# Performance work log

Hardware: AMD Instinct MI355X
Metric: run time of the kernel (lower is better)

## Reference

```python
import jax, jax.numpy as jnp
import numpy as np
from jax import lax

B, T = 8192, 2048
INIT_ALPHA = 0.1


def setup_inputs() -> dict:
    key = jax.random.key(0)
    kx, = jax.random.split(key, 1)
    # intermittent demand: small non-negative integers, many exact zeros
    x = jax.random.randint(kx, (B, T), 0, 3).astype(jnp.float32)
    alpha = jnp.full((1, 1), INIT_ALPHA, dtype=jnp.float32)  # learned smoothing weight
    Z0 = jnp.ones((B,), dtype=jnp.float32)  # demand-size state
    V0 = jnp.ones((B,), dtype=jnp.float32)  # inter-demand-interval state
    q0 = jnp.ones((B,), dtype=jnp.float32)  # periods since last nonzero demand
    return {"x": x, "alpha": alpha, "Z0": Z0, "V0": V0, "q0": q0}


def reference(x, alpha, Z0, V0, q0):
    """Croston's method recurrence (sba=False): out_t = Z_t / V_t.

    x: (B, T) demand series; states are per-series scalars carried through a scan.
    """
    a = alpha[0, 0]

    def step(carry, xt):  # xt: (B,)
        Z, V, q = carry
        Z_next = a * xt + (1.0 - a) * Z
        V_next = a * q + (1.0 - a) * V
        nz = xt != 0.0
        Z_next = jnp.where(nz, Z_next, Z)
        V_next = jnp.where(nz, V_next, V)
        q_next = jnp.where(nz, 1.0, q + 1.0)
        out = Z_next / V_next  # sba=False branch
        return (Z_next, V_next, q_next), out

    _, outs = lax.scan(step, (Z0, V0, q0), x.T)  # outs: (T, B)
    return outs.T  # (B, T)
```

## Files before the change

kernel.cpp:

```cpp
#include <hip/hip_runtime.h>
#include <stdint.h>


#define TLEN 2048

typedef float vf4 __attribute__((ext_vector_type(4)));

__global__ __launch_bounds__(256) void croston_kernel(
    const float* __restrict__ x,
    const float* __restrict__ alpha,
    const float* __restrict__ Z0,
    const float* __restrict__ V0,
    const float* __restrict__ q0,
    float* __restrict__ out)
{
    __shared__ __attribute__((aligned(16))) float lds[4][2048];

    const int warp = threadIdx.x >> 6;
    const int lane = threadIdx.x & 63;
    const int wid  = blockIdx.x * 4 + warp;
    float* W = lds[warp];

    const float a  = alpha[0];
    const float ma = 1.0f - a;

    const int e  = (lane & 7) ^ ((lane >> 3) & 7);
    const int l7 = lane & 7;

    const float* row = x + (size_t)wid * TLEN;
    vf4 ld[8];
#pragma unroll
    for (int j = 0; j < 8; ++j)
        ld[j] = *(const vf4*)(row + j * 256 + lane * 4);

#pragma unroll
    for (int j = 0; j < 8; ++j)
        *(vf4*)(W + (j * 8 + (lane >> 3)) * 32 + (e << 2)) = ld[j];

    vf4 xv[8];
#pragma unroll
    for (int m = 0; m < 8; ++m)
        xv[m] = *(const vf4*)(W + lane * 32 + ((m ^ l7) << 2));

    float az = 1.f, bz = 0.f;
    float p  = 1.f, r = 0.f, s = 0.f;
    float f  = 1.f, g = 0.f;
#pragma unroll
    for (int j = 0; j < 8; ++j) {
#pragma unroll
        for (int k = 0; k < 4; ++k) {
            const float xt = xv[j][k];
            const bool  nz = (xt != 0.f);
            const float az_n = ma * az;
            const float bz_n = fmaf(ma, bz, a * xt);
            const float p_n  = ma * p;
            const float r_n  = fmaf(ma, r, a * f);
            const float s_n  = fmaf(ma, s, a * g);
            az = nz ? az_n : az;
            bz = nz ? bz_n : bz;
            p  = nz ? p_n  : p;
            r  = nz ? r_n  : r;
            s  = nz ? s_n  : s;
            g  = nz ? 1.f  : (g + 1.f);
            f  = nz ? 0.f  : f;
        }
    }

#pragma unroll
    for (int d = 1; d < 64; d <<= 1) {
        const float az_o = __shfl_up(az, d);
        const float bz_o = __shfl_up(bz, d);
        const float p_o  = __shfl_up(p,  d);
        const float r_o  = __shfl_up(r,  d);
        const float s_o  = __shfl_up(s,  d);
        const float f_o  = __shfl_up(f,  d);
        const float g_o  = __shfl_up(g,  d);
        if (lane >= d) {
            bz = fmaf(az, bz_o, bz);
            az = az * az_o;
            s  = fmaf(p, s_o, fmaf(r, g_o, s));
            r  = fmaf(p, r_o, r * f_o);
            p  = p * p_o;
            g  = fmaf(f, g_o, g);
            f  = f * f_o;
        }
    }

    float azE = __shfl_up(az, 1), bzE = __shfl_up(bz, 1);
    float pE  = __shfl_up(p, 1),  rE  = __shfl_up(r, 1), sE = __shfl_up(s, 1);
    float fE  = __shfl_up(f, 1),  gE  = __shfl_up(g, 1);
    if (lane == 0) {
        azE = 1.f; bzE = 0.f;
        pE  = 1.f; rE  = 0.f; sE = 0.f;
        fE  = 1.f; gE  = 0.f;
    }

    const float z0  = Z0[wid];
    const float v0  = V0[wid];
    const float qq0 = q0[wid];
    float Z = fmaf(azE, z0, bzE);
    float V = fmaf(pE, v0, fmaf(rE, qq0, sE));
    float q = fmaf(fE, qq0, gE);

#pragma unroll
    for (int j = 0; j < 8; ++j) {
#pragma unroll
        for (int k = 0; k < 4; ++k) {
            const float xt = xv[j][k];
            const bool  nz = (xt != 0.f);
            const float Zn = fmaf(ma, Z, a * xt);
            const float Vn = fmaf(ma, V, a * q);
            Z = nz ? Zn : Z;
            V = nz ? Vn : V;
            q = nz ? 1.f : (q + 1.f);
            xv[j][k] = Z * __builtin_amdgcn_rcpf(V);
        }
    }

#pragma unroll
    for (int m = 0; m < 8; ++m)
        *(vf4*)(W + lane * 32 + ((m ^ l7) << 2)) = xv[m];

    float* orow = out + (size_t)wid * TLEN;
#pragma unroll
    for (int j = 0; j < 8; ++j) {
        vf4 o = *(const vf4*)(W + (j * 8 + (lane >> 3)) * 32 + (e << 2));
        *(vf4*)(orow + j * 256 + lane * 4) = o;
    }
}

extern "C" void kernel_launch(void* const* d_in, const int* in_sizes, int n_in,
                              void* d_out, int out_size, void* d_ws, size_t ws_size,
                              hipStream_t stream) {
    const float* x     = (const float*)d_in[0];
    const float* alpha = (const float*)d_in[1];
    const float* Z0    = (const float*)d_in[2];
    const float* V0    = (const float*)d_in[3];
    const float* q0    = (const float*)d_in[4];
    float* out = (float*)d_out;

    dim3 block(256);
    dim3 grid(2048);
    croston_kernel<<<grid, block, 0, stream>>>(x, alpha, Z0, V0, q0, out);
}
```

Baseline: 118.8 us.

## Process each row in two halves with prefetch overlapping scan

Splits each wavefront's 2048-element row into two 1024-element halves, each scanned with its own wave-wide prefix combine, and carries the end state between halves. The second half's global loads are issued before the first half's scan, so memory latency overlaps compute. Halving the LDS buffer lets more blocks fit per CU, and since p always equals az in the scan, that state variable is dropped. In exchange there is a second shuffle-scan pass and extra shuffles to broadcast the end state.

```diff
diff --git a/kernel.cpp b/kernel.cpp
--- a/kernel.cpp
+++ b/kernel.cpp
@@ -3,6 +3,7 @@
 
 
 #define TLEN 2048
+#define HALF 1024
 
 typedef float vf4 __attribute__((ext_vector_type(4)));
 
@@ -14,7 +15,7 @@
     const float* __restrict__ q0,
     float* __restrict__ out)
 {
-    __shared__ __attribute__((aligned(16))) float lds[4][2048];
+    __shared__ __attribute__((aligned(16))) float lds[4][HALF];
 
     const int warp = threadIdx.x >> 6;
     const int lane = threadIdx.x & 63;
@@ -24,108 +25,134 @@
     const float a  = alpha[0];
     const float ma = 1.0f - a;
 
-    const int e  = (lane & 7) ^ ((lane >> 3) & 7);
-    const int l7 = lane & 7;
+    const int rg  = lane >> 3;
+    const int pqg = ((((lane >> 2) & 1) << 2) | (lane & 3)) ^ ((lane >> 3) & 7);
+    const int goff = rg * 32 + pqg * 4;
 
-    const float* row = x + (size_t)wid * TLEN;
-    vf4 ld[8];
+    const int rowl = lane >> 1;
+    const int lbase = rowl * 32;
+    const int lkey  = rowl & 7;
+    const int lhalf = (lane & 1) << 2;
+
+    auto lane_off = [&](int m) { return lbase + (((lhalf | m) ^ lkey) << 2); };
+
+    auto scan_half = [&](vf4* xv, float& Zs, float& Vs, float& qs) {
+        float az = 1.f, bz = 0.f, r = 0.f, s = 0.f, f = 1.f, g = 0.f;
 #pragma unroll
-    for (int j = 0; j < 8; ++j)
+        for (int m = 0; m < 4; ++m) {
+#pragma unroll
+            for (int k = 0; k < 4; ++k) {
+                const float xt = xv[m][k];
+                const bool  nz = (xt != 0.f);
+                const float az_n = ma * az;
+                const float bz_n = fmaf(ma, bz, a * xt);
+                const float r_n  = fmaf(ma, r, a * f);
+                const float s_n  = fmaf(ma, s, a * g);
+                az = nz ? az_n : az;
+                bz = nz ? bz_n : bz;
+                r  = nz ? r_n  : r;
+                s  = nz ? s_n  : s;
+                g  = nz ? 1.f  : (g + 1.f);
+                f  = nz ? 0.f  : f;
+            }
+        }
+#pragma unroll
+        for (int d = 1; d < 64; d <<= 1) {
+            const float az_o = __shfl_up(az, d);
+            const float bz_o = __shfl_up(bz, d);
+            const float r_o  = __shfl_up(r,  d);
+            const float s_o  = __shfl_up(s,  d);
+            const float f_o  = __shfl_up(f,  d);
+            const float g_o  = __shfl_up(g,  d);
+            if (lane >= d) {
+                bz = fmaf(az, bz_o, bz);
+                s  = fmaf(az, s_o, fmaf(r, g_o, s));
+                r  = fmaf(az, r_o, r * f_o);
+                az = az * az_o;
+                g  = fmaf(f, g_o, g);
+                f  = f * f_o;
+            }
+        }
+        const float azT = __shfl(az, 63), bzT = __shfl(bz, 63);
+        const float rT  = __shfl(r, 63),  sT  = __shfl(s, 63);
+        const float fT  = __shfl(f, 63),  gT  = __shfl(g, 63);
+        const float Ze = fmaf(azT, Zs, bzT);
+        const float Ve = fmaf(azT, Vs, fmaf(rT, qs, sT));
+        const float qe = fmaf(fT, qs, gT);
+        float azE = __shfl_up(az, 1), bzE = __shfl_up(bz, 1);
+        float rE  = __shfl_up(r, 1),  sE  = __shfl_up(s, 1);
+        float fE  = __shfl_up(f, 1),  gE  = __shfl_up(g, 1);
+        if (lane == 0) {
+            azE = 1.f; bzE = 0.f; rE = 0.f; sE = 0.f; fE = 1.f; gE = 0.f;
+        }
+        float Z = fmaf(azE, Zs, bzE);
+        float V = fmaf(azE, Vs, fmaf(rE, qs, sE));
+        float q = fmaf(fE, qs, gE);
+#pragma unroll
+        for (int m = 0; m < 4; ++m) {
+#pragma unroll
+            for (int k = 0; k < 4; ++k) {
+                const float xt = xv[m][k];
+                const bool  nz = (xt != 0.f);
+                const float Zn = fmaf(ma, Z, a * xt);
+                const float Vn = fmaf(ma, V, a * q);
+                Z = nz ? Zn : Z;
+                V = nz ? Vn : V;
+                q = nz ? 1.f : (q + 1.f);
+                xv[m][k] = Z * __builtin_amdgcn_rcpf(V);
+            }
+        }
+        Zs = Ze; Vs = Ve; qs = qe;
+    };
+
+    const float* row  = x   + (size_t)wid * TLEN;
+    float*       orow = out + (size_t)wid * TLEN;
+
+    float Zs = Z0[wid], Vs = V0[wid], qs = q0[wid];
+
+    vf4 ld[4];
+#pragma unroll
+    for (int j = 0; j < 4; ++j)
         ld[j] = *(const vf4*)(row + j * 256 + lane * 4);
+#pragma unroll
+    for (int j = 0; j < 4; ++j)
+        *(vf4*)(W + j * 256 + goff) = ld[j];
+    vf4 xv[4];
+#pragma unroll
+    for (int m = 0; m < 4; ++m)
+        xv[m] = *(const vf4*)(W + lane_off(m));
 
 #pragma unroll
-    for (int j = 0; j < 8; ++j)
-        *(vf4*)(W + (j * 8 + (lane >> 3)) * 32 + (e << 2)) = ld[j];
+    for (int j = 0; j < 4; ++j)
+        ld[j] = *(const vf4*)(row + HALF + j * 256 + lane * 4);
 
-    vf4 xv[8];
+    scan_half(xv, Zs, Vs, qs);
+
 #pragma unroll
-    for (int m = 0; m < 8; ++m)
-        xv[m] = *(const vf4*)(W + lane * 32 + ((m ^ l7) << 2));
-
-    float az = 1.f, bz = 0.f;
-    float p  = 1.f, r = 0.f, s = 0.f;
-    float f  = 1.f, g = 0.f;
+    for (int m = 0; m < 4; ++m)
+        *(vf4*)(W + lane_off(m)) = xv[m];
 #pragma unroll
-    for (int j = 0; j < 8; ++j) {
-#pragma unroll
-        for (int k = 0; k < 4; ++k) {
-            const float xt = xv[j][k];
-            const bool  nz = (xt != 0.f);
-            const float az_n = ma * az;
-            const float bz_n = fmaf(ma, bz, a * xt);
-            const float p_n  = ma * p;
-            const float r_n  = fmaf(ma, r, a * f);
-            const float s_n  = fmaf(ma, s, a * g);
-            az = nz ? az_n : az;
-            bz = nz ? bz_n : bz;
-            p  = nz ? p_n  : p;
-            r  = nz ? r_n  : r;
-            s  = nz ? s_n  : s;
-            g  = nz ? 1.f  : (g + 1.f);
-            f  = nz ? 0.f  : f;
-        }
+    for (int j = 0; j < 4; ++j) {
+        const vf4 o = *(const vf4*)(W + j * 256 + goff);
+        *(vf4*)(orow + j * 256 + lane * 4) = o;
     }
 
 #pragma unroll
-    for (int d = 1; d < 64; d <<= 1) {
-        const float az_o = __shfl_up(az, d);
-        const float bz_o = __shfl_up(bz, d);
-        const float p_o  = __shfl_up(p,  d);
-        const float r_o  = __shfl_up(r,  d);
-        const float s_o  = __shfl_up(s,  d);
-        const float f_o  = __shfl_up(f,  d);
-        const float g_o  = __shfl_up(g,  d);
-        if (lane >= d) {
-            bz = fmaf(az, bz_o, bz);
-            az = az * az_o;
-            s  = fmaf(p, s_o, fmaf(r, g_o, s));
-            r  = fmaf(p, r_o, r * f_o);
-            p  = p * p_o;
-            g  = fmaf(f, g_o, g);
-            f  = f * f_o;
-        }
-    }
+    for (int j = 0; j < 4; ++j)
+        *(vf4*)(W + j * 256 + goff) = ld[j];
+#pragma unroll
+    for (int m = 0; m < 4; ++m)
+        xv[m] = *(const vf4*)(W + lane_off(m));
 
-    float azE = __shfl_up(az, 1), bzE = __shfl_up(bz, 1);
-    float pE  = __shfl_up(p, 1),  rE  = __shfl_up(r, 1), sE = __shfl_up(s, 1);
-    float fE  = __shfl_up(f, 1),  gE  = __shfl_up(g, 1);
-    if (lane == 0) {
-        azE = 1.f; bzE = 0.f;
-        pE  = 1.f; rE  = 0.f; sE = 0.f;
-        fE  = 1.f; gE  = 0.f;
-    }
-
-    const float z0  = Z0[wid];
-    const float v0  = V0[wid];
-    const float qq0 = q0[wid];
-    float Z = fmaf(azE, z0, bzE);
-    float V = fmaf(pE, v0, fmaf(rE, qq0, sE));
-    float q = fmaf(fE, qq0, gE);
+    scan_half(xv, Zs, Vs, qs);
 
 #pragma unroll
-    for (int j = 0; j < 8; ++j) {
+    for (int m = 0; m < 4; ++m)
+        *(vf4*)(W + lane_off(m)) = xv[m];
 #pragma unroll
-        for (int k = 0; k < 4; ++k) {
-            const float xt = xv[j][k];
-            const bool  nz = (xt != 0.f);
-            const float Zn = fmaf(ma, Z, a * xt);
-            const float Vn = fmaf(ma, V, a * q);
-            Z = nz ? Zn : Z;
-            V = nz ? Vn : V;
-            q = nz ? 1.f : (q + 1.f);
-            xv[j][k] = Z * __builtin_amdgcn_rcpf(V);
-        }
-    }
-
-#pragma unroll
-    for (int m = 0; m < 8; ++m)
-        *(vf4*)(W + lane * 32 + ((m ^ l7) << 2)) = xv[m];
-
-    float* orow = out + (size_t)wid * TLEN;
-#pragma unroll
-    for (int j = 0; j < 8; ++j) {
-        vf4 o = *(const vf4*)(W + (j * 8 + (lane >> 3)) * 32 + (e << 2));
-        *(vf4*)(orow + j * 256 + lane * 4) = o;
+    for (int j = 0; j < 4; ++j) {
+        const vf4 o = *(const vf4*)(W + j * 256 + goff);
+        *(vf4*)(orow + HALF + j * 256 + lane * 4) = o;
     }
 }
 
```

New measurement: 118.2 us, median of 2. Within noise of the previous version (-0.5%).

## Process four rows per wave with double-buffered register prefetch of next row

Applied to the files above, without the earlier changes.

Each wave now handles four consecutive series instead of one, and the grid shrinks from 2048 to 512 blocks. The next row's global loads are issued into a second register buffer before the current row's scan runs, so load latency overlaps with compute. The p state is dropped because it always equals az, which removes one shuffle and its multiplies from each scan step. Register pressure rises from the double buffer, and fewer waves reduce latency hiding from occupancy. The code relies on in-order LDS reuse within a wave and places no barrier between rows.

```diff
diff --git a/kernel.cpp b/kernel.cpp
--- a/kernel.cpp
+++ b/kernel.cpp
@@ -18,114 +18,123 @@
 
     const int warp = threadIdx.x >> 6;
     const int lane = threadIdx.x & 63;
-    const int wid  = blockIdx.x * 4 + warp;
+    const int wave = blockIdx.x * 4 + warp;
+    const int wid0 = wave * 4;
     float* W = lds[warp];
 
     const float a  = alpha[0];
     const float ma = 1.0f - a;
 
-    const int e  = (lane & 7) ^ ((lane >> 3) & 7);
-    const int l7 = lane & 7;
+    const int rg   = lane >> 3;
+    const int e    = (lane & 7) ^ rg;
+    const int goff = rg * 32 + (e << 2);
+    const int l7   = lane & 7;
+    const int lbase = lane * 32;
 
-    const float* row = x + (size_t)wid * TLEN;
-    vf4 ld[8];
+    float zs[4], vs[4], qsx[4];
+#pragma unroll
+    for (int i = 0; i < 4; ++i) {
+        zs[i]  = Z0[wid0 + i];
+        vs[i]  = V0[wid0 + i];
+        qsx[i] = q0[wid0 + i];
+    }
+
+    vf4 buf[2][8];
 #pragma unroll
     for (int j = 0; j < 8; ++j)
-        ld[j] = *(const vf4*)(row + j * 256 + lane * 4);
+        buf[0][j] = *(const vf4*)(x + (size_t)wid0 * TLEN + j * 256 + lane * 4);
 
 #pragma unroll
-    for (int j = 0; j < 8; ++j)
-        *(vf4*)(W + (j * 8 + (lane >> 3)) * 32 + (e << 2)) = ld[j];
+    for (int i = 0; i < 4; ++i) {
+        const int wid = wid0 + i;
 
-    vf4 xv[8];
+        if (i < 3) {
 #pragma unroll
-    for (int m = 0; m < 8; ++m)
-        xv[m] = *(const vf4*)(W + lane * 32 + ((m ^ l7) << 2));
-
-    float az = 1.f, bz = 0.f;
-    float p  = 1.f, r = 0.f, s = 0.f;
-    float f  = 1.f, g = 0.f;
-#pragma unroll
-    for (int j = 0; j < 8; ++j) {
-#pragma unroll
-        for (int k = 0; k < 4; ++k) {
-            const float xt = xv[j][k];
-            const bool  nz = (xt != 0.f);
-            const float az_n = ma * az;
-            const float bz_n = fmaf(ma, bz, a * xt);
-            const float p_n  = ma * p;
-            const float r_n  = fmaf(ma, r, a * f);
-            const float s_n  = fmaf(ma, s, a * g);
-            az = nz ? az_n : az;
-            bz = nz ? bz_n : bz;
-            p  = nz ? p_n  : p;
-            r  = nz ? r_n  : r;
-            s  = nz ? s_n  : s;
-            g  = nz ? 1.f  : (g + 1.f);
-            f  = nz ? 0.f  : f;
+            for (int j = 0; j < 8; ++j)
+                buf[(i + 1) & 1][j] =
+                    *(const vf4*)(x + (size_t)(wid + 1) * TLEN + j * 256 + lane * 4);
         }
-    }
 
 #pragma unroll
-    for (int d = 1; d < 64; d <<= 1) {
-        const float az_o = __shfl_up(az, d);
-        const float bz_o = __shfl_up(bz, d);
-        const float p_o  = __shfl_up(p,  d);
-        const float r_o  = __shfl_up(r,  d);
-        const float s_o  = __shfl_up(s,  d);
-        const float f_o  = __shfl_up(f,  d);
-        const float g_o  = __shfl_up(g,  d);
-        if (lane >= d) {
-            bz = fmaf(az, bz_o, bz);
-            az = az * az_o;
-            s  = fmaf(p, s_o, fmaf(r, g_o, s));
-            r  = fmaf(p, r_o, r * f_o);
-            p  = p * p_o;
-            g  = fmaf(f, g_o, g);
-            f  = f * f_o;
+        for (int j = 0; j < 8; ++j)
+            *(vf4*)(W + j * 256 + goff) = buf[i & 1][j];
+        vf4 xv[8];
+#pragma unroll
+        for (int m = 0; m < 8; ++m)
+            xv[m] = *(const vf4*)(W + lbase + ((m ^ l7) << 2));
+
+        float az = 1.f, bz = 0.f, r = 0.f, s = 0.f, f = 1.f, g = 0.f;
+#pragma unroll
+        for (int m = 0; m < 8; ++m) {
+#pragma unroll
+            for (int k = 0; k < 4; ++k) {
+                const float xt = xv[m][k];
+                const bool  nz = (xt != 0.f);
+                const float az_n = ma * az;
+                const float bz_n = fmaf(ma, bz, a * xt);
+                const float r_n  = fmaf(ma, r, a * f);
+                const float s_n  = fmaf(ma, s, a * g);
+                az = nz ? az_n : az;
+                bz = nz ? bz_n : bz;
+                r  = nz ? r_n  : r;
+                s  = nz ? s_n  : s;
+                g  = nz ? 1.f  : (g + 1.f);
+                f  = nz ? 0.f  : f;
+            }
         }
-    }
-
-    float azE = __shfl_up(az, 1), bzE = __shfl_up(bz, 1);
-    float pE  = __shfl_up(p, 1),  rE  = __shfl_up(r, 1), sE = __shfl_up(s, 1);
-    float fE  = __shfl_up(f, 1),  gE  = __shfl_up(g, 1);
-    if (lane == 0) {
-        azE = 1.f; bzE = 0.f;
-        pE  = 1.f; rE  = 0.f; sE = 0.f;
-        fE  = 1.f; gE  = 0.f;
-    }
-
-    const float z0  = Z0[wid];
-    const float v0  = V0[wid];
-    const float qq0 = q0[wid];
-    float Z = fmaf(azE, z0, bzE);
-    float V = fmaf(pE, v0, fmaf(rE, qq0, sE));
-    float q = fmaf(fE, qq0, gE);
 
 #pragma unroll
-    for (int j = 0; j < 8; ++j) {
-#pragma unroll
-        for (int k = 0; k < 4; ++k) {
-            const float xt = xv[j][k];
-            const bool  nz = (xt != 0.f);
-            const float Zn = fmaf(ma, Z, a * xt);
-            const float Vn = fmaf(ma, V, a * q);
-            Z = nz ? Zn : Z;
-            V = nz ? Vn : V;
-            q = nz ? 1.f : (q + 1.f);
-            xv[j][k] = Z * __builtin_amdgcn_rcpf(V);
+        for (int d = 1; d < 64; d <<= 1) {
+            const float az_o = __shfl_up(az, d);
+            const float bz_o = __shfl_up(bz, d);
+            const float r_o  = __shfl_up(r,  d);
+            const float s_o  = __shfl_up(s,  d);
+            const float f_o  = __shfl_up(f,  d);
+            const float g_o  = __shfl_up(g,  d);
+            if (lane >= d) {
+                bz = fmaf(az, bz_o, bz);
+                s  = fmaf(az, s_o, fmaf(r, g_o, s));
+                r  = fmaf(az, r_o, r * f_o);
+                az = az * az_o;
+                g  = fmaf(f, g_o, g);
+                f  = f * f_o;
+            }
         }
-    }
+
+        float azE = __shfl_up(az, 1), bzE = __shfl_up(bz, 1);
+        float rE  = __shfl_up(r, 1),  sE  = __shfl_up(s, 1);
+        float fE  = __shfl_up(f, 1),  gE  = __shfl_up(g, 1);
+        if (lane == 0) {
+            azE = 1.f; bzE = 0.f; rE = 0.f; sE = 0.f; fE = 1.f; gE = 0.f;
+        }
+
+        float Z = fmaf(azE, zs[i], bzE);
+        float V = fmaf(azE, vs[i], fmaf(rE, qsx[i], sE));
+        float q = fmaf(fE, qsx[i], gE);
 
 #pragma unroll
-    for (int m = 0; m < 8; ++m)
-        *(vf4*)(W + lane * 32 + ((m ^ l7) << 2)) = xv[m];
+        for (int m = 0; m < 8; ++m) {
+#pragma unroll
+            for (int k = 0; k < 4; ++k) {
+                const float xt = xv[m][k];
+                const bool  nz = (xt != 0.f);
+                const float Zn = fmaf(ma, Z, a * xt);
+                const float Vn = fmaf(ma, V, a * q);
+                Z = nz ? Zn : Z;
+                V = nz ? Vn : V;
+                q = nz ? 1.f : (q + 1.f);
+                xv[m][k] = Z * __builtin_amdgcn_rcpf(V);
+            }
+        }
 
-    float* orow = out + (size_t)wid * TLEN;
 #pragma unroll
-    for (int j = 0; j < 8; ++j) {
-        vf4 o = *(const vf4*)(W + (j * 8 + (lane >> 3)) * 32 + (e << 2));
-        *(vf4*)(orow + j * 256 + lane * 4) = o;
+        for (int m = 0; m < 8; ++m)
+            *(vf4*)(W + lbase + ((m ^ l7) << 2)) = xv[m];
+#pragma unroll
+        for (int j = 0; j < 8; ++j) {
+            const vf4 o = *(const vf4*)(W + j * 256 + goff);
+            *(vf4*)(out + (size_t)wid * TLEN + j * 256 + lane * 4) = o;
+        }
     }
 }
 
@@ -140,6 +149,6 @@
     float* out = (float*)d_out;
 
     dim3 block(256);
-    dim3 grid(2048);
+    dim3 grid(512);
     croston_kernel<<<grid, block, 0, stream>>>(x, alpha, Z0, V0, q0, out);
 }
```

New measurement: 119.8 us. Within noise of the previous version (+0.8%).
